# Kernel tuning notes

Measured on AMD Instinct MI355X. Metric: run time of the kernel, lower is better.

## Reference

```python
import jax, jax.numpy as jnp
import numpy as np

N = 30000
E = 300000
F_IN = 512
OUT = 1024


def _l2norm(x):
    # F.normalize(x, p=2, dim=1) with eps=1e-12
    n = jnp.linalg.norm(x, axis=1, keepdims=True)
    return x / jnp.maximum(n, 1e-12)


def _gcn_conv(x, W, b, row, col, w):
    # PyG GCNConv: x' = D^-1/2 (A + I) D^-1/2 (x W) + b, self-loops weight 1
    n = x.shape[0]
    h = x @ W  # [n, out]
    deg = jax.ops.segment_sum(w, row, num_segments=n)
    dinv = jnp.where(deg > 0, jax.lax.rsqrt(deg), 0.0)
    nw = dinv[row] * w * dinv[col]  # per-edge norm
    agg = jax.ops.segment_sum(h[col] * nw[:, None], row, num_segments=n)
    return agg + b


def _forward(x, edge_index, edge_weight, beta,
             W1, b1, W2, b2, W3, b3, Wmu, bmu, Wlv, blv, Wd1, bd1, Wd2, bd2):
    n = x.shape[0]
    loops = jnp.arange(n, dtype=edge_index.dtype)
    row = jnp.concatenate([edge_index[0], loops])
    col = jnp.concatenate([edge_index[1], loops])
    w = jnp.concatenate([edge_weight, jnp.ones((n,), edge_weight.dtype)])

    out1 = jax.nn.relu(_l2norm(_gcn_conv(x, W1, b1, row, col, w)))
    out2 = jax.nn.relu(_l2norm(_gcn_conv(out1, W2, b2, row, col, w)))
    out3 = jax.nn.relu(_l2norm(_gcn_conv(out2, W3, b3, row, col, w)))

    mu = out3 @ Wmu + bmu
    logvar = out3 @ Wlv + blv

    # reparameterize(mu, beta * logvar) with eps ~ N(0,1)*0.01
    lv = beta * logvar
    std = jnp.exp(0.5 * lv)
    eps = jax.random.normal(jax.random.key(42), std.shape, std.dtype) * 0.01
    z = mu + eps * std

    # batch=None pooling: global max + mean over nodes
    pooled = jnp.concatenate([jnp.max(z, axis=0), jnp.mean(z, axis=0)])[None, :]  # [1, 1024]

    h = jax.nn.relu(pooled @ Wd1 + bd1)
    recon_x = jax.nn.sigmoid(h @ Wd2 + bd2)
    return recon_x, mu, logvar


def setup_inputs() -> dict:
    key = jax.random.key(0)
    ks = jax.random.split(key, 20)
    def glorot(k, shape):
        lim = np.sqrt(6.0 / (shape[0] + shape[1]))
        return jax.random.uniform(k, shape, jnp.float32, -lim, lim)
    H = 512
    return {
        "x": jax.random.normal(ks[0], (N, F_IN), jnp.float32),
        "edge_index": jax.random.randint(ks[1], (2, E), 0, N, jnp.int64),
        "edge_weight": jax.random.uniform(ks[2], (E,), jnp.float32),
        "beta": 1,
        "W1": glorot(ks[3], (F_IN, 1024)), "b1": jnp.zeros((1024,), jnp.float32),
        "W2": glorot(ks[4], (1024, 512)), "b2": jnp.zeros((512,), jnp.float32),
        "W3": glorot(ks[5], (512, 256)), "b3": jnp.zeros((256,), jnp.float32),
        "Wmu": glorot(ks[6], (256, H)), "bmu": jnp.zeros((H,), jnp.float32),
        "Wlv": glorot(ks[7], (256, H)), "blv": jnp.zeros((H,), jnp.float32),
        "Wd1": glorot(ks[8], (2 * H, 2 * H)), "bd1": jnp.zeros((2 * H,), jnp.float32),
        "Wd2": glorot(ks[9], (2 * H, OUT)), "bd2": jnp.zeros((OUT,), jnp.float32),
    }


def reference(x, edge_index, edge_weight, beta,
              W1, b1, W2, b2, W3, b3, Wmu, bmu, Wlv, blv, Wd1, bd1, Wd2, bd2):
    return _forward(x, edge_index, edge_weight, beta,
                    W1, b1, W2, b2, W3, b3, Wmu, bmu, Wlv, blv, Wd1, bd1, Wd2, bd2)
```

## Files before the change

kernel.cpp:

```cpp
#include <hip/hip_runtime.h>
#include <cstdint>
#include <cstddef>

#define NNODE      30000
#define FIN        512
#define H1DIM      1024
#define H2DIM      512
#define H3DIM      256
#define HDIM       512
#define HALF_ROWS  15000
#define HALF_ELEMS 7680000u
#define PP_ROWS    16
#define PP_BLOCKS  938
#define PM_BLOCKS  64
#define MPANELS    240

typedef __attribute__((ext_vector_type(8))) short s16x8;
typedef __attribute__((ext_vector_type(4))) short s16x4;
typedef __attribute__((ext_vector_type(4))) float f32x4;

__device__ __forceinline__ short f2bf(float f) {
    uint32_t u = __float_as_uint(f);
    uint32_t r = (u + 0x7FFFu + ((u >> 16) & 1u)) >> 16;
    return (short)r;
}
__device__ __forceinline__ float bf2f(short s) {
    return __uint_as_float(((uint32_t)(uint16_t)s) << 16);
}

__device__ __forceinline__ void threefry2x32(uint32_t k0, uint32_t k1,
                                             uint32_t& x0, uint32_t& x1) {
    uint32_t ks0 = k0, ks1 = k1, ks2 = k0 ^ k1 ^ 0x1BD11BDAu;
    const uint32_t R0[4] = {13u, 15u, 26u, 6u};
    const uint32_t R1[4] = {17u, 29u, 16u, 24u};
    x0 += ks0; x1 += ks1;
#pragma unroll
    for (int g = 0; g < 5; ++g) {
        const uint32_t* R = (g & 1) ? R1 : R0;
#pragma unroll
        for (int r = 0; r < 4; ++r) {
            x0 += x1;
            x1 = (x1 << R[r]) | (x1 >> (32u - R[r]));
            x1 ^= x0;
        }
        uint32_t ks_a = (g % 3 == 0) ? ks1 : (g % 3 == 1 ? ks2 : ks0);
        uint32_t ks_b = (g % 3 == 0) ? ks2 : (g % 3 == 1 ? ks0 : ks1);
        x0 += ks_a;
        x1 += ks_b + (uint32_t)(g + 1);
    }
}

__device__ __forceinline__ float jax_normal(uint32_t bits) {
    uint32_t fb = (bits >> 9) | 0x3F800000u;
    float f = __uint_as_float(fb) - 1.0f;
    const float lo = -0.99999994f;
    float u = fmaf(f, 2.0f, lo);
    u = fmaxf(u, lo);
    return 1.41421356237f * erfinvf(u);
}

__global__ void deg_cnt_kernel(const int* __restrict__ row, const float* __restrict__ w,
                               float* __restrict__ deg, int* __restrict__ cnt, int E) {
    int e = blockIdx.x * 256 + threadIdx.x;
    if (e < E) {
        int r = row[e];
        atomicAdd(&deg[r], w[e]);
        atomicAdd(&cnt[r], 1);
    }
}

__global__ void dinv_kernel(const float* __restrict__ deg, float* __restrict__ dinv, int n) {
    int i = blockIdx.x * 256 + threadIdx.x;
    if (i < n) dinv[i] = rsqrtf(deg[i] + 1.0f);
}

__global__ void rsqrt_clamp_kernel(float* __restrict__ ss, int n) {
    int i = blockIdx.x * 256 + threadIdx.x;
    if (i < n) ss[i] = 1.0f / fmaxf(sqrtf(ss[i]), 1e-12f);
}

__global__ __launch_bounds__(256) void build_rowptr(const int* __restrict__ cnt,
                                                    int* __restrict__ rowptr) {
    __shared__ int sums[256];
    const int ROWS_PT = 118;
    int t = threadIdx.x;
    int base = t * ROWS_PT;
    int local = 0;
    for (int i = 0; i < ROWS_PT; ++i) {
        int r = base + i;
        if (r < NNODE) local += cnt[r];
    }
    sums[t] = local;
    __syncthreads();
    for (int o = 1; o < 256; o <<= 1) {
        int v = (t >= o) ? sums[t - o] : 0;
        __syncthreads();
        sums[t] += v;
        __syncthreads();
    }
    int off = (t == 0) ? 0 : sums[t - 1];
    for (int i = 0; i < ROWS_PT; ++i) {
        int r = base + i;
        if (r < NNODE) { rowptr[r] = off; off += cnt[r]; }
    }
    if (t == 255) rowptr[NNODE] = off;
}

__global__ void scatter_edges(const int* __restrict__ row, const int* __restrict__ col,
                              const float* __restrict__ w, const float* __restrict__ dinv,
                              const int* __restrict__ rowptr, int* __restrict__ fill,
                              int* __restrict__ ecol, float* __restrict__ eval, int E) {
    int e = blockIdx.x * 256 + threadIdx.x;
    if (e < E) {
        int r = row[e], c = col[e];
        int pos = rowptr[r] + atomicAdd(&fill[r], 1);
        ecol[pos] = c;
        eval[pos] = dinv[r] * w[e] * dinv[c];
    }
}

__global__ void f32_to_bf16(const float* __restrict__ in, short* __restrict__ out, int n4) {
    int i = blockIdx.x * 256 + threadIdx.x;
    if (i < n4) {
        float4 v = ((const float4*)in)[i];
        s16x4 s = { f2bf(v.x), f2bf(v.y), f2bf(v.z), f2bf(v.w) };
        *(s16x4*)(out + (size_t)i * 4) = s;
    }
}

__global__ __launch_bounds__(256) void transpose_bf16(const float* __restrict__ W,
                                                      short* __restrict__ Wt, int K, int N) {
    __shared__ float t[32][33];
    int kb = blockIdx.y * 32, nb = blockIdx.x * 32;
    int tx = threadIdx.x & 31, ty = threadIdx.x >> 5;
#pragma unroll
    for (int i = 0; i < 32; i += 8)
        if (kb + ty + i < K && nb + tx < N)
            t[ty + i][tx] = W[(size_t)(kb + ty + i) * N + nb + tx];
    __syncthreads();
#pragma unroll
    for (int i = 0; i < 32; i += 8)
        if (nb + ty + i < N && kb + tx < K)
            Wt[(size_t)(nb + ty + i) * K + kb + tx] = f2bf(t[tx][ty + i]);
}

template <int F, bool FUSE>
__global__ __launch_bounds__(256) void spmm_bf16(const int* __restrict__ rowptr,
                                                 const int* __restrict__ ecol,
                                                 const float* __restrict__ eval,
                                                 const float* __restrict__ dinv,
                                                 const short* __restrict__ h,
                                                 const float* __restrict__ bias,
                                                 short* __restrict__ out) {
    constexpr int NE = F / 64;
    int lane = threadIdx.x & 63;
    int r = blockIdx.x * 4 + (threadIdx.x >> 6);
    if (r >= NNODE) return;
    float d = dinv[r];
    float dd = d * d;
    float acc[NE];
    {
        const short* p = h + (size_t)r * F + lane * NE;
        if constexpr (NE == 8) {
            s16x8 v = *(const s16x8*)p;
#pragma unroll
            for (int j = 0; j < 8; ++j) acc[j] = dd * bf2f(v[j]);
        } else {
            s16x4 v = *(const s16x4*)p;
#pragma unroll
            for (int j = 0; j < 4; ++j) acc[j] = dd * bf2f(v[j]);
        }
    }
    int e0 = rowptr[r], e1 = rowptr[r + 1];
    int e = e0;
    for (; e + 2 <= e1; e += 2) {
        int c0 = ecol[e], c1 = ecol[e + 1];
        float w0 = eval[e], w1 = eval[e + 1];
        const short* p0 = h + (size_t)c0 * F + lane * NE;
        const short* p1 = h + (size_t)c1 * F + lane * NE;
        if constexpr (NE == 8) {
            s16x8 v0 = *(const s16x8*)p0;
            s16x8 v1 = *(const s16x8*)p1;
#pragma unroll
            for (int j = 0; j < 8; ++j) acc[j] = fmaf(w0, bf2f(v0[j]), acc[j]);
#pragma unroll
            for (int j = 0; j < 8; ++j) acc[j] = fmaf(w1, bf2f(v1[j]), acc[j]);
        } else {
            s16x4 v0 = *(const s16x4*)p0;
            s16x4 v1 = *(const s16x4*)p1;
#pragma unroll
            for (int j = 0; j < 4; ++j) acc[j] = fmaf(w0, bf2f(v0[j]), acc[j]);
#pragma unroll
            for (int j = 0; j < 4; ++j) acc[j] = fmaf(w1, bf2f(v1[j]), acc[j]);
        }
    }
    if (e < e1) {
        int c = ecol[e];
        float nw = eval[e];
        const short* p = h + (size_t)c * F + lane * NE;
        if constexpr (NE == 8) {
            s16x8 v = *(const s16x8*)p;
#pragma unroll
            for (int j = 0; j < 8; ++j) acc[j] = fmaf(nw, bf2f(v[j]), acc[j]);
        } else {
            s16x4 v = *(const s16x4*)p;
#pragma unroll
            for (int j = 0; j < 4; ++j) acc[j] = fmaf(nw, bf2f(v[j]), acc[j]);
        }
    }
    short* o = out + (size_t)r * F + lane * NE;
    if (FUSE) {
        const float* bp = bias + lane * NE;
        float ss = 0.f;
#pragma unroll
        for (int j = 0; j < NE; ++j) { acc[j] += bp[j]; ss += acc[j] * acc[j]; }
#pragma unroll
        for (int off = 32; off; off >>= 1) ss += __shfl_xor(ss, off);
        float rinv = 1.0f / fmaxf(sqrtf(ss), 1e-12f);
#pragma unroll
        for (int j = 0; j < NE; ++j) acc[j] = fmaxf(acc[j] * rinv, 0.f);
    }
    if constexpr (NE == 8) {
        s16x8 s;
#pragma unroll
        for (int j = 0; j < 8; ++j) s[j] = f2bf(acc[j]);
        *(s16x8*)o = s;
    } else {
        s16x4 s;
#pragma unroll
        for (int j = 0; j < 4; ++j) s[j] = f2bf(acc[j]);
        *(s16x4*)o = s;
    }
}

template <typename OutT, bool ADD_BIAS, int EPI>
__global__ __launch_bounds__(256) void gemm_bf16(const short* __restrict__ A,
                                                 const short* __restrict__ Bt,
                                                 const float* __restrict__ bias,
                                                 const float* __restrict__ bias2,
                                                 OutT* __restrict__ C,
                                                 float* __restrict__ C2,
                                                 float* __restrict__ ssbuf,
                                                 int M, int N, int K) {
    __shared__ short sA[128 * 64];
    __shared__ short sB[128 * 64];
    const int tid = threadIdx.x;
    const int lane = tid & 63;
    const int w = tid >> 6;
    const int wm = w >> 1, wn = w & 1;

    const int nx = N >> 7;
    const int lg = __builtin_ctz(nx);
    const int lin = blockIdx.x;
    const int low = lin & 7;
    const int t = lin >> 3;
    const int cblk = t & (nx - 1);
    const int pid = ((t >> lg) << 3) + low;
    const int m0 = pid << 7;
    if (m0 >= M) return;
    const int n0 = cblk << 7;

    const int srow = lane >> 3;
    const int scol = ((lane & 7) ^ srow) * 8;

    f32x4 acc[4][4] = {};

    const int lrow = lane & 15;
    const int jhi = lane >> 4;

    const int nkt = K >> 6;
    for (int kt = 0; kt < nkt; ++kt) {
        const int k0 = kt << 6;
#pragma unroll
        for (int i = 0; i < 4; ++i) {
            int c = i * 4 + w;
            int tr = c * 8 + srow;
            __builtin_amdgcn_global_load_lds(
                (const __attribute__((address_space(1))) void*)(A + (size_t)(m0 + tr) * K + k0 + scol),
                (__attribute__((address_space(3))) void*)(sA + c * 512),
                16, 0, 0);
        }
#pragma unroll
        for (int i = 0; i < 4; ++i) {
            int c = i * 4 + w;
            int tr = c * 8 + srow;
            __builtin_amdgcn_global_load_lds(
                (const __attribute__((address_space(1))) void*)(Bt + (size_t)(n0 + tr) * K + k0 + scol),
                (__attribute__((address_space(3))) void*)(sB + c * 512),
                16, 0, 0);
        }
        __syncthreads();

        s16x8 af[4][2], bfr[4][2];
#pragma unroll
        for (int fm = 0; fm < 4; ++fm) {
            int lr = wm * 64 + fm * 16 + lrow;
            const short* base = &sA[lr * 64];
            int sl0 = jhi ^ (lr & 7);
            af[fm][0] = *(const s16x8*)&base[sl0 << 3];
            af[fm][1] = *(const s16x8*)&base[(sl0 ^ 4) << 3];
        }
#pragma unroll
        for (int fn = 0; fn < 4; ++fn) {
            int lr = wn * 64 + fn * 16 + lrow;
            const short* base = &sB[lr * 64];
            int sl0 = jhi ^ (lr & 7);
            bfr[fn][0] = *(const s16x8*)&base[sl0 << 3];
            bfr[fn][1] = *(const s16x8*)&base[(sl0 ^ 4) << 3];
        }
#pragma unroll
        for (int fm = 0; fm < 4; ++fm)
#pragma unroll
            for (int fn = 0; fn < 4; ++fn) {
                acc[fm][fn] = __builtin_amdgcn_mfma_f32_16x16x32_bf16(af[fm][0], bfr[fn][0], acc[fm][fn], 0, 0, 0);
                acc[fm][fn] = __builtin_amdgcn_mfma_f32_16x16x32_bf16(af[fm][1], bfr[fn][1], acc[fm][fn], 0, 0, 0);
            }
        __syncthreads();
    }

    const int crow = (lane >> 4) * 4;
    const int ccol = lane & 15;

    if constexpr (EPI == 1) {
        float ssl[4][4] = {};
#pragma unroll
        for (int fm = 0; fm < 4; ++fm) {
#pragma unroll
            for (int fn = 0; fn < 4; ++fn) {
                int n = n0 + wn * 64 + fn * 16 + ccol;
                float b = bias[n];
#pragma unroll
                for (int r = 0; r < 4; ++r) {
                    float o = acc[fm][fn][r] + b;
                    ssl[fm][r] += o * o;
                    int m = m0 + wm * 64 + fm * 16 + crow + r;
                    if (m < M) C[(size_t)m * N + n] = (OutT)f2bf(fmaxf(o, 0.f));
                }
            }
        }
#pragma unroll
        for (int fm = 0; fm < 4; ++fm)
#pragma unroll
            for (int r = 0; r < 4; ++r) {
                float v = ssl[fm][r];
                v += __shfl_xor(v, 1); v += __shfl_xor(v, 2);
                v += __shfl_xor(v, 4); v += __shfl_xor(v, 8);
                int m = m0 + wm * 64 + fm * 16 + crow + r;
                if (ccol == 0 && m < M) atomicAdd(&ssbuf[m], v);
            }
    } else if constexpr (EPI == 2) {
#pragma unroll
        for (int fm = 0; fm < 4; ++fm) {
#pragma unroll
            for (int fn = 0; fn < 4; ++fn) {
                int n = n0 + wn * 64 + fn * 16 + ccol;
#pragma unroll
                for (int r = 0; r < 4; ++r) {
                    int m = m0 + wm * 64 + fm * 16 + crow + r;
                    if (m < M) {
                        float sc = ssbuf[m];
                        C[(size_t)m * N + n] = (OutT)f2bf(acc[fm][fn][r] * sc);
                    }
                }
            }
        }
    } else if constexpr (EPI == 3) {
        const int half = N >> 1;
#pragma unroll
        for (int fm = 0; fm < 4; ++fm) {
#pragma unroll
            for (int fn = 0; fn < 4; ++fn) {
                int n = n0 + wn * 64 + fn * 16 + ccol;
                bool hi = n >= half;
                float b = hi ? bias2[n - half] : bias[n];
                float* Cp = hi ? C2 : (float*)C;
                int nc = hi ? (n - half) : n;
#pragma unroll
                for (int r = 0; r < 4; ++r) {
                    int m = m0 + wm * 64 + fm * 16 + crow + r;
                    if (m < M) Cp[(size_t)m * half + nc] = acc[fm][fn][r] + b;
                }
            }
        }
    } else {
#pragma unroll
        for (int fm = 0; fm < 4; ++fm) {
#pragma unroll
            for (int fn = 0; fn < 4; ++fn) {
                int n = n0 + wn * 64 + fn * 16 + ccol;
                float b = ADD_BIAS ? bias[n] : 0.f;
#pragma unroll
                for (int r = 0; r < 4; ++r) {
                    int m = m0 + wm * 64 + fm * 16 + crow + r;
                    if (m < M) {
                        float o = acc[fm][fn][r] + b;
                        if constexpr (sizeof(OutT) == 2) C[(size_t)m * N + n] = (OutT)f2bf(o);
                        else                             C[(size_t)m * N + n] = o;
                    }
                }
            }
        }
    }
}

__global__ __launch_bounds__(256) void pool_partial(const float* __restrict__ mu,
                                                    const float* __restrict__ lv,
                                                    const uint32_t* __restrict__ beta_p,
                                                    float* __restrict__ pmax,
                                                    float* __restrict__ psum) {
    uint32_t bb = beta_p[0];
    float beta = (bb & 0x7F800000u) ? __uint_as_float(bb) : (float)(int)bb;
    int b = blockIdx.x;
    int r0 = b * PP_ROWS;
    int r1 = min(r0 + PP_ROWS, HALF_ROWS);
    int c = threadIdx.x * 2;
    float m0 = -INFINITY, m1 = -INFINITY, s0 = 0.f, s1 = 0.f;
    for (int r = r0; r < r1; ++r) {
        size_t ia = (size_t)r * HDIM + c;
        size_t ib = (size_t)(r + HALF_ROWS) * HDIM + c;
        float2 mua = *(const float2*)&mu[ia];
        float2 lva = *(const float2*)&lv[ia];
        float2 mub = *(const float2*)&mu[ib];
        float2 lvb = *(const float2*)&lv[ib];
        uint32_t idx0 = (uint32_t)r * 512u + (uint32_t)c;
        uint32_t xa0 = idx0,     ya0 = idx0 + HALF_ELEMS;
        uint32_t xa1 = idx0 + 1, ya1 = idx0 + 1 + HALF_ELEMS;
        threefry2x32(0u, 42u, xa0, ya0);
        threefry2x32(0u, 42u, xa1, ya1);
        float za0 = mua.x + 0.01f * jax_normal(xa0) * __expf(0.5f * beta * lva.x);
        float zb0 = mub.x + 0.01f * jax_normal(ya0) * __expf(0.5f * beta * lvb.x);
        float za1 = mua.y + 0.01f * jax_normal(xa1) * __expf(0.5f * beta * lva.y);
        float zb1 = mub.y + 0.01f * jax_normal(ya1) * __expf(0.5f * beta * lvb.y);
        m0 = fmaxf(m0, fmaxf(za0, zb0)); s0 += za0 + zb0;
        m1 = fmaxf(m1, fmaxf(za1, zb1)); s1 += za1 + zb1;
    }
    pmax[(size_t)b * HDIM + c]     = m0;
    pmax[(size_t)b * HDIM + c + 1] = m1;
    psum[(size_t)b * HDIM + c]     = s0;
    psum[(size_t)b * HDIM + c + 1] = s1;
}

__global__ __launch_bounds__(256) void pool_mid(const float* __restrict__ pmax,
                                                const float* __restrict__ psum,
                                                float* __restrict__ pmax2,
                                                float* __restrict__ psum2) {
    int g = blockIdx.x;
    int b0 = g * 15;
    int b1 = min(b0 + 15, PP_BLOCKS);
#pragma unroll
    for (int pass = 0; pass < 2; ++pass) {
        int c = threadIdx.x + pass * 256;
        float m = -INFINITY, s = 0.f;
        for (int b = b0; b < b1; ++b) {
            m = fmaxf(m, pmax[(size_t)b * HDIM + c]);
            s += psum[(size_t)b * HDIM + c];
        }
        pmax2[(size_t)g * HDIM + c] = m;
        psum2[(size_t)g * HDIM + c] = s;
    }
}

__global__ void pool_final(const float* __restrict__ pmax2, const float* __restrict__ psum2,
                           float* __restrict__ pooled) {
    int c = blockIdx.x * 256 + threadIdx.x;
    if (c < HDIM) {
        float m = -INFINITY, s = 0.f;
#pragma unroll
        for (int b = 0; b < PM_BLOCKS; ++b) {
            m = fmaxf(m, pmax2[(size_t)b * HDIM + c]);
            s += psum2[(size_t)b * HDIM + c];
        }
        pooled[c] = m;
        pooled[HDIM + c] = s / 30000.0f;
    }
}

__global__ __launch_bounds__(256) void dense_partial(const float* __restrict__ in,
                                                     const float* __restrict__ W,
                                                     float* __restrict__ part) {
    int by = blockIdx.y;
    int j = blockIdx.x * 256 + threadIdx.x;
    __shared__ float sin_[128];
    if (threadIdx.x < 128) sin_[threadIdx.x] = in[by * 128 + threadIdx.x];
    __syncthreads();
    float acc = 0.f;
#pragma unroll 8
    for (int i = 0; i < 128; ++i)
        acc = fmaf(sin_[i], W[(size_t)(by * 128 + i) * 1024 + j], acc);
    part[(size_t)by * 1024 + j] = acc;
}

__global__ void dense_final(const float* __restrict__ part, const float* __restrict__ bias,
                            float* __restrict__ out, int act) {
    int j = blockIdx.x * 256 + threadIdx.x;
    float acc = bias[j];
#pragma unroll
    for (int s = 0; s < 8; ++s) acc += part[(size_t)s * 1024 + j];
    out[j] = act ? (1.0f / (1.0f + __expf(-acc))) : fmaxf(acc, 0.f);
}

extern "C" void kernel_launch(void* const* d_in, const int* in_sizes, int n_in,
                              void* d_out, int out_size, void* d_ws, size_t ws_size,
                              hipStream_t stream) {
    const float* x   = (const float*)d_in[0];
    const int*   ei  = (const int*)d_in[1];
    const float* ew  = (const float*)d_in[2];
    const uint32_t* beta = (const uint32_t*)d_in[3];
    const float* W1  = (const float*)d_in[4];
    const float* b1  = (const float*)d_in[5];
    const float* W2  = (const float*)d_in[6];
    const float* b2  = (const float*)d_in[7];
    const float* W3  = (const float*)d_in[8];
    const float* b3  = (const float*)d_in[9];
    const float* Wmu = (const float*)d_in[10];
    const float* bmu = (const float*)d_in[11];
    const float* Wlv = (const float*)d_in[12];
    const float* blv = (const float*)d_in[13];
    const float* Wd1 = (const float*)d_in[14];
    const float* bd1 = (const float*)d_in[15];
    const float* Wd2 = (const float*)d_in[16];
    const float* bd2 = (const float*)d_in[17];

    const int E = in_sizes[2];
    const int M = NNODE;

    float* out    = (float*)d_out;
    float* mu_out = out + 1024;
    float* lv_out = out + 1024 + (size_t)M * HDIM;

    char* Wp = (char*)d_ws;
    short* slotA  = (short*)(Wp);
    short* slotB  = (short*)(Wp + 61603840);
    short* xb     = (short*)(Wp + 123207680);
    short* W1t    = (short*)(Wp + 154009600);
    short* W2t    = (short*)(Wp + 155058176);
    short* W3t    = (short*)(Wp + 156106752);
    short* Wmut   = (short*)(Wp + 156368896);
    short* Wlvt   = (short*)(Wp + 156631040);
    float* deg    = (float*)(Wp + 156893184);
    float* dinv   = (float*)(Wp + 157013184);
    int*   cnt    = (int*)  (Wp + 157133184);
    int*   fill   = (int*)  (Wp + 157253184);
    float* ssbuf  = (float*)(Wp + 157373184);
    int*   rowptr = (int*)  (Wp + 157493184);
    int*   ecol   = (int*)  (Wp + 157613188);
    float* eval   = (float*)(Wp + 158813188);
    float* pmax   = (float*)(Wp + 160013188);
    float* psum   = (float*)(Wp + 161934212);
    float* pmax2  = (float*)(Wp + 163855236);
    float* psum2  = (float*)(Wp + 163986308);
    float* pooled = (float*)(Wp + 164117380);
    float* hdec   = (float*)(Wp + 164121476);
    float* dpart  = (float*)(Wp + 164125572);

    const int* row = ei;
    const int* col = ei + E;

    hipMemsetAsync(deg, 0, 600000, stream);

    deg_cnt_kernel<<<(E + 255) / 256, 256, 0, stream>>>(row, ew, deg, cnt, E);
    dinv_kernel<<<(M + 255) / 256, 256, 0, stream>>>(deg, dinv, M);
    build_rowptr<<<1, 256, 0, stream>>>(cnt, rowptr);
    scatter_edges<<<(E + 255) / 256, 256, 0, stream>>>(row, col, ew, dinv, rowptr, fill,
                                                       ecol, eval, E);

    f32_to_bf16<<<(M * FIN / 4 + 255) / 256, 256, 0, stream>>>(x, xb, M * FIN / 4);
    {
        dim3 b(256);
        transpose_bf16<<<dim3(H1DIM / 32, FIN / 32),   b, 0, stream>>>(W1,  W1t,  FIN,   H1DIM);
        transpose_bf16<<<dim3(H2DIM / 32, H1DIM / 32), b, 0, stream>>>(W2,  W2t,  H1DIM, H2DIM);
        transpose_bf16<<<dim3(H3DIM / 32, H2DIM / 32), b, 0, stream>>>(W3,  W3t,  H2DIM, H3DIM);
        transpose_bf16<<<dim3(HDIM / 32,  H3DIM / 32), b, 0, stream>>>(Wmu, Wmut, H3DIM, HDIM);
        transpose_bf16<<<dim3(HDIM / 32,  H3DIM / 32), b, 0, stream>>>(Wlv, Wlvt, H3DIM, HDIM);
    }

    const int SPMM_GRID = (M + 3) / 4;

    spmm_bf16<512, false><<<SPMM_GRID, 256, 0, stream>>>(rowptr, ecol, eval, dinv, xb,
                                                         nullptr, slotA);
    gemm_bf16<short, true, 1><<<(H1DIM / 128) * MPANELS, 256, 0, stream>>>(
        slotA, W1t, b1, nullptr, slotB, nullptr, ssbuf, M, H1DIM, FIN);
    rsqrt_clamp_kernel<<<(M + 255) / 256, 256, 0, stream>>>(ssbuf, M);

    gemm_bf16<short, false, 2><<<(H2DIM / 128) * MPANELS, 256, 0, stream>>>(
        slotB, W2t, nullptr, nullptr, slotA, nullptr, ssbuf, M, H2DIM, H1DIM);
    spmm_bf16<512, true><<<SPMM_GRID, 256, 0, stream>>>(rowptr, ecol, eval, dinv, slotA,
                                                        b2, slotB);

    gemm_bf16<short, false, 0><<<(H3DIM / 128) * MPANELS, 256, 0, stream>>>(
        slotB, W3t, nullptr, nullptr, slotA, nullptr, nullptr, M, H3DIM, H2DIM);
    spmm_bf16<256, true><<<SPMM_GRID, 256, 0, stream>>>(rowptr, ecol, eval, dinv, slotA,
                                                        b3, slotB);

    gemm_bf16<float, true, 3><<<((2 * HDIM) / 128) * MPANELS, 256, 0, stream>>>(
        slotB, Wmut, bmu, blv, mu_out, lv_out, nullptr, M, 2 * HDIM, H3DIM);

    pool_partial<<<PP_BLOCKS, 256, 0, stream>>>(mu_out, lv_out, beta, pmax, psum);
    pool_mid<<<PM_BLOCKS, 256, 0, stream>>>(pmax, psum, pmax2, psum2);
    pool_final<<<2, 256, 0, stream>>>(pmax2, psum2, pooled);

    dense_partial<<<dim3(4, 8), 256, 0, stream>>>(pooled, Wd1, dpart);
    dense_final<<<4, 256, 0, stream>>>(dpart, bd1, hdec, 0);
    dense_partial<<<dim3(4, 8), 256, 0, stream>>>(hdec, Wd2, dpart);
    dense_final<<<4, 256, 0, stream>>>(dpart, bd2, out, 1);
}
```

Baseline: 532.8 us.

## Double-buffer GEMM tiles with 256-row blocks, XCD remap, and parallel rowptr scan

The bf16 GEMM now uses 512-thread blocks with 256x128 output tiles and double-buffered LDS, so the next K tile is prefetched while MFMAs run on the current one. Blocks are remapped so that consecutive tiles land on the same XCD, which is meant to improve L2 reuse. The single-block rowptr prefix sum is split into a block-sum, a scan and a write kernel so it runs on many CUs. The GEMM uses 96KB of LDS, which limits occupancy, and it drops the m0>=M guard, relying on 118 panels of 256 rows plus buffer padding to cover the 30000 rows.

```diff
diff --git a/kernel.cpp b/kernel.cpp
--- a/kernel.cpp
+++ b/kernel.cpp
@@ -13,7 +13,8 @@
 #define PP_ROWS    16
 #define PP_BLOCKS  938
 #define PM_BLOCKS  64
-#define MPANELS    240
+#define NPANEL     118
+#define NSCAN      118
 
 typedef __attribute__((ext_vector_type(8))) short s16x8;
 typedef __attribute__((ext_vector_type(4))) short s16x4;
@@ -79,31 +80,49 @@
     if (i < n) ss[i] = 1.0f / fmaxf(sqrtf(ss[i]), 1e-12f);
 }
 
-__global__ __launch_bounds__(256) void build_rowptr(const int* __restrict__ cnt,
-                                                    int* __restrict__ rowptr) {
-    __shared__ int sums[256];
-    const int ROWS_PT = 118;
+__global__ __launch_bounds__(256) void rp_blocksum(const int* __restrict__ cnt,
+                                                   int* __restrict__ bsum) {
+    __shared__ int sh[256];
+    int i = blockIdx.x * 256 + threadIdx.x;
+    sh[threadIdx.x] = (i < NNODE) ? cnt[i] : 0;
+    __syncthreads();
+    for (int o = 128; o; o >>= 1) {
+        if (threadIdx.x < o) sh[threadIdx.x] += sh[threadIdx.x + o];
+        __syncthreads();
+    }
+    if (threadIdx.x == 0) bsum[blockIdx.x] = sh[0];
+}
+
+__global__ __launch_bounds__(128) void rp_scan(int* __restrict__ bsum, int nb) {
+    __shared__ int sh[128];
     int t = threadIdx.x;
-    int base = t * ROWS_PT;
-    int local = 0;
-    for (int i = 0; i < ROWS_PT; ++i) {
-        int r = base + i;
-        if (r < NNODE) local += cnt[r];
-    }
-    sums[t] = local;
+    sh[t] = (t < nb) ? bsum[t] : 0;
+    __syncthreads();
+    for (int o = 1; o < 128; o <<= 1) {
+        int v = (t >= o) ? sh[t - o] : 0;
+        __syncthreads();
+        sh[t] += v;
+        __syncthreads();
+    }
+    if (t < nb) bsum[t] = (t == 0) ? 0 : sh[t - 1];
+}
+
+__global__ __launch_bounds__(256) void rp_write(const int* __restrict__ cnt,
+                                                const int* __restrict__ bsum,
+                                                int* __restrict__ rowptr, int E) {
+    __shared__ int sh[256];
+    int i = blockIdx.x * 256 + threadIdx.x;
+    int v = (i < NNODE) ? cnt[i] : 0;
+    sh[threadIdx.x] = v;
     __syncthreads();
     for (int o = 1; o < 256; o <<= 1) {
-        int v = (t >= o) ? sums[t - o] : 0;
+        int x = (threadIdx.x >= o) ? sh[threadIdx.x - o] : 0;
         __syncthreads();
-        sums[t] += v;
+        sh[threadIdx.x] += x;
         __syncthreads();
     }
-    int off = (t == 0) ? 0 : sums[t - 1];
-    for (int i = 0; i < ROWS_PT; ++i) {
-        int r = base + i;
-        if (r < NNODE) { rowptr[r] = off; off += cnt[r]; }
-    }
-    if (t == 255) rowptr[NNODE] = off;
+    if (i < NNODE) rowptr[i] = bsum[blockIdx.x] + sh[threadIdx.x] - v;
+    if (i == NNODE - 1) rowptr[NNODE] = E;
 }
 
 __global__ void scatter_edges(const int* __restrict__ row, const int* __restrict__ col,
@@ -233,8 +252,29 @@
     }
 }
 
+#define STAGE_TILE(buf_, kt_)                                                              \
+  {                                                                                        \
+    const int k0_ = (kt_) << 6;                                                            \
+    _Pragma("unroll")                                                                      \
+    for (int i_ = 0; i_ < 4; ++i_) {                                                       \
+      int c_ = i_ * 8 + w;                                                                 \
+      int tr_ = c_ * 8 + srow;                                                             \
+      __builtin_amdgcn_global_load_lds(                                                    \
+          (const __attribute__((address_space(1))) void*)(A + (size_t)(m0 + tr_) * K + k0_ + scol), \
+          (__attribute__((address_space(3))) void*)(&sA[buf_][c_ * 512]), 16, 0, 0);       \
+    }                                                                                      \
+    _Pragma("unroll")                                                                      \
+    for (int i_ = 0; i_ < 2; ++i_) {                                                       \
+      int c_ = i_ * 8 + w;                                                                 \
+      int tr_ = c_ * 8 + srow;                                                             \
+      __builtin_amdgcn_global_load_lds(                                                    \
+          (const __attribute__((address_space(1))) void*)(Bt + (size_t)(n0 + tr_) * K + k0_ + scol), \
+          (__attribute__((address_space(3))) void*)(&sB[buf_][c_ * 512]), 16, 0, 0);       \
+    }                                                                                      \
+  }
+
 template <typename OutT, bool ADD_BIAS, int EPI>
-__global__ __launch_bounds__(256) void gemm_bf16(const short* __restrict__ A,
+__global__ __launch_bounds__(512) void gemm_bf16(const short* __restrict__ A,
                                                  const short* __restrict__ Bt,
                                                  const float* __restrict__ bias,
                                                  const float* __restrict__ bias2,
@@ -242,22 +282,24 @@
                                                  float* __restrict__ C2,
                                                  float* __restrict__ ssbuf,
                                                  int M, int N, int K) {
-    __shared__ short sA[128 * 64];
-    __shared__ short sB[128 * 64];
+    __shared__ short sA[2][256 * 64];
+    __shared__ short sB[2][128 * 64];
     const int tid = threadIdx.x;
     const int lane = tid & 63;
     const int w = tid >> 6;
     const int wm = w >> 1, wn = w & 1;
 
+    const int nwg = gridDim.x;
+    const int orig = blockIdx.x;
+    const int q = nwg >> 3, rr = nwg & 7;
+    const int xcd = orig & 7;
+    const int base = (xcd < rr) ? xcd * (q + 1) : rr * (q + 1) + (xcd - rr) * q;
+    const int wgid = base + (orig >> 3);
     const int nx = N >> 7;
     const int lg = __builtin_ctz(nx);
-    const int lin = blockIdx.x;
-    const int low = lin & 7;
-    const int t = lin >> 3;
-    const int cblk = t & (nx - 1);
-    const int pid = ((t >> lg) << 3) + low;
-    const int m0 = pid << 7;
-    if (m0 >= M) return;
+    const int pid = wgid >> lg;
+    const int cblk = wgid & (nx - 1);
+    const int m0 = pid << 8;
     const int n0 = cblk << 7;
 
     const int srow = lane >> 3;
@@ -269,53 +311,37 @@
     const int jhi = lane >> 4;
 
     const int nkt = K >> 6;
+    int cur = 0;
+    STAGE_TILE(0, 0);
+    __syncthreads();
+
     for (int kt = 0; kt < nkt; ++kt) {
-        const int k0 = kt << 6;
-#pragma unroll
-        for (int i = 0; i < 4; ++i) {
-            int c = i * 4 + w;
-            int tr = c * 8 + srow;
-            __builtin_amdgcn_global_load_lds(
-                (const __attribute__((address_space(1))) void*)(A + (size_t)(m0 + tr) * K + k0 + scol),
-                (__attribute__((address_space(3))) void*)(sA + c * 512),
-                16, 0, 0);
-        }
-#pragma unroll
-        for (int i = 0; i < 4; ++i) {
-            int c = i * 4 + w;
-            int tr = c * 8 + srow;
-            __builtin_amdgcn_global_load_lds(
-                (const __attribute__((address_space(1))) void*)(Bt + (size_t)(n0 + tr) * K + k0 + scol),
-                (__attribute__((address_space(3))) void*)(sB + c * 512),
-                16, 0, 0);
-        }
-        __syncthreads();
-
-        s16x8 af[4][2], bfr[4][2];
+        if (kt + 1 < nkt) STAGE_TILE(cur ^ 1, kt + 1);
+
+        s16x8 bfr[4][2];
+#pragma unroll
+        for (int fn = 0; fn < 4; ++fn) {
+            int lr = wn * 64 + fn * 16 + lrow;
+            const short* bptr = &sB[cur][lr * 64];
+            int sl0 = jhi ^ (lr & 7);
+            bfr[fn][0] = *(const s16x8*)&bptr[sl0 << 3];
+            bfr[fn][1] = *(const s16x8*)&bptr[(sl0 ^ 4) << 3];
+        }
 #pragma unroll
         for (int fm = 0; fm < 4; ++fm) {
             int lr = wm * 64 + fm * 16 + lrow;
-            const short* base = &sA[lr * 64];
+            const short* aptr = &sA[cur][lr * 64];
             int sl0 = jhi ^ (lr & 7);
-            af[fm][0] = *(const s16x8*)&base[sl0 << 3];
-            af[fm][1] = *(const s16x8*)&base[(sl0 ^ 4) << 3];
-        }
-#pragma unroll
-        for (int fn = 0; fn < 4; ++fn) {
-            int lr = wn * 64 + fn * 16 + lrow;
-            const short* base = &sB[lr * 64];
-            int sl0 = jhi ^ (lr & 7);
-            bfr[fn][0] = *(const s16x8*)&base[sl0 << 3];
-            bfr[fn][1] = *(const s16x8*)&base[(sl0 ^ 4) << 3];
-        }
-#pragma unroll
-        for (int fm = 0; fm < 4; ++fm)
+            s16x8 a0 = *(const s16x8*)&aptr[sl0 << 3];
+            s16x8 a1 = *(const s16x8*)&aptr[(sl0 ^ 4) << 3];
 #pragma unroll
             for (int fn = 0; fn < 4; ++fn) {
-                acc[fm][fn] = __builtin_amdgcn_mfma_f32_16x16x32_bf16(af[fm][0], bfr[fn][0], acc[fm][fn], 0, 0, 0);
-                acc[fm][fn] = __builtin_amdgcn_mfma_f32_16x16x32_bf16(af[fm][1], bfr[fn][1], acc[fm][fn], 0, 0, 0);
+                acc[fm][fn] = __builtin_amdgcn_mfma_f32_16x16x32_bf16(a0, bfr[fn][0], acc[fm][fn], 0, 0, 0);
+                acc[fm][fn] = __builtin_amdgcn_mfma_f32_16x16x32_bf16(a1, bfr[fn][1], acc[fm][fn], 0, 0, 0);
             }
+        }
         __syncthreads();
+        cur ^= 1;
     }
 
     const int crow = (lane >> 4) * 4;
@@ -552,6 +578,7 @@
     float* pooled = (float*)(Wp + 164117380);
     float* hdec   = (float*)(Wp + 164121476);
     float* dpart  = (float*)(Wp + 164125572);
+    int*   bsum   = (int*)pmax;
 
     const int* row = ei;
     const int* col = ei + E;
@@ -560,7 +587,9 @@
 
     deg_cnt_kernel<<<(E + 255) / 256, 256, 0, stream>>>(row, ew, deg, cnt, E);
     dinv_kernel<<<(M + 255) / 256, 256, 0, stream>>>(deg, dinv, M);
-    build_rowptr<<<1, 256, 0, stream>>>(cnt, rowptr);
+    rp_blocksum<<<NSCAN, 256, 0, stream>>>(cnt, bsum);
+    rp_scan<<<1, 128, 0, stream>>>(bsum, NSCAN);
+    rp_write<<<NSCAN, 256, 0, stream>>>(cnt, bsum, rowptr, E);
     scatter_edges<<<(E + 255) / 256, 256, 0, stream>>>(row, col, ew, dinv, rowptr, fill,
                                                        ecol, eval, E);
 
@@ -578,21 +607,21 @@
 
     spmm_bf16<512, false><<<SPMM_GRID, 256, 0, stream>>>(rowptr, ecol, eval, dinv, xb,
                                                          nullptr, slotA);
-    gemm_bf16<short, true, 1><<<(H1DIM / 128) * MPANELS, 256, 0, stream>>>(
+    gemm_bf16<short, true, 1><<<(H1DIM / 128) * NPANEL, 512, 0, stream>>>(
         slotA, W1t, b1, nullptr, slotB, nullptr, ssbuf, M, H1DIM, FIN);
     rsqrt_clamp_kernel<<<(M + 255) / 256, 256, 0, stream>>>(ssbuf, M);
 
-    gemm_bf16<short, false, 2><<<(H2DIM / 128) * MPANELS, 256, 0, stream>>>(
+    gemm_bf16<short, false, 2><<<(H2DIM / 128) * NPANEL, 512, 0, stream>>>(
         slotB, W2t, nullptr, nullptr, slotA, nullptr, ssbuf, M, H2DIM, H1DIM);
     spmm_bf16<512, true><<<SPMM_GRID, 256, 0, stream>>>(rowptr, ecol, eval, dinv, slotA,
                                                         b2, slotB);
 
-    gemm_bf16<short, false, 0><<<(H3DIM / 128) * MPANELS, 256, 0, stream>>>(
+    gemm_bf16<short, false, 0><<<(H3DIM / 128) * NPANEL, 512, 0, stream>>>(
         slotB, W3t, nullptr, nullptr, slotA, nullptr, nullptr, M, H3DIM, H2DIM);
     spmm_bf16<256, true><<<SPMM_GRID, 256, 0, stream>>>(rowptr, ecol, eval, dinv, slotA,
                                                         b3, slotB);
 
-    gemm_bf16<float, true, 3><<<((2 * HDIM) / 128) * MPANELS, 256, 0, stream>>>(
+    gemm_bf16<float, true, 3><<<((2 * HDIM) / 128) * NPANEL, 512, 0, stream>>>(
         slotB, Wmut, bmu, blv, mu_out, lv_out, nullptr, M, 2 * HDIM, H3DIM);
 
     pool_partial<<<PP_BLOCKS, 256, 0, stream>>>(mu_out, lv_out, beta, pmax, psum);
```

After: 506.5 us. 1.05x faster.
